# Kernel optimization log

Hardware: AMD Instinct MI355X
Metric: run time of the kernel (lower is better)

Reference implementation:

```python
import jax, jax.numpy as jnp
import numpy as np

MULTIRES = 6          # positional-encoding frequencies (get_embedder)
SKIP_LAYER = 4        # skip_in=(4,) in ImplicitNetwork
BETA = 100.0          # Softplus(beta=100)
INV_SQRT2 = float(1.0 / np.sqrt(2.0))
NUM_NETS = 64         # multi displacement networks (clusters)


def embed(x):
    """NeRF positional embedding: [x, sin(2^k x), cos(2^k x)] for k=0..MULTIRES-1.
    x: [N,3] -> [N, 3 + 3*2*MULTIRES] = [N,39]."""
    outs = [x]
    for i in range(MULTIRES):
        f = float(2.0 ** i)
        outs.append(jnp.sin(f * x))
        outs.append(jnp.cos(f * x))
    return jnp.concatenate(outs, axis=-1)


def softplus100(x):
    # numerically stable softplus with beta=100
    return jnp.logaddexp(0.0, BETA * x) / BETA


def _forward(points,
             iW0, ib0, iW1, ib1, iW2, ib2, iW3, ib3, iW4, ib4,
             iW5, ib5, iW6, ib6, iW7, ib7, iW8, ib8,
             dW0, db0, dW1, db1, dW2, db2, dW3, db3,
             mW0, mb0, mW1, mb1, mW2, mb2):
    N = points.shape[0]
    inp = embed(points)  # [N,39]

    # ---- ImplicitNetwork: 9 linears, softplus(beta=100), skip concat at l=4 ----
    iWs = [iW0, iW1, iW2, iW3, iW4, iW5, iW6, iW7, iW8]
    ibs = [ib0, ib1, ib2, ib3, ib4, ib5, ib6, ib7, ib8]
    x = inp
    for l in range(9):
        if l == SKIP_LAYER:
            x = jnp.concatenate([x, inp], axis=1) * INV_SQRT2  # [N,473+39=512]
        x = x @ iWs[l].T + ibs[l]
        if l < 8:
            x = softplus100(x)
    sdf_feat = x  # [N,257] = sdf (1) + feature vector (256)

    # ---- DisplacementNetwork: 4 linears, ReLU on hidden, Tanh output ----
    xd = inp
    for W, b, last in ((dW0, db0, False), (dW1, db1, False), (dW2, db2, False), (dW3, db3, True)):
        xd = xd @ W.T + b
        xd = jnp.tanh(xd) if last else jax.nn.relu(xd)
    disp = xd  # [N,3]

    # ---- MultiDisplacementNetwork: batched per-cluster MLPs via bmm ----
    xm = inp.reshape(NUM_NETS, -1, inp.shape[1])  # [n, N/n, 39]
    xm = jax.nn.relu(jnp.einsum('nbi,noi->nbo', xm, mW0) + mb0[:, None, :])
    xm = jax.nn.relu(jnp.einsum('nbi,noi->nbo', xm, mW1) + mb1[:, None, :])
    xm = jnp.tanh(jnp.einsum('nbi,noi->nbo', xm, mW2) + mb2[:, None, :])
    mdisp = xm.reshape(N, 3)

    return jnp.concatenate([sdf_feat, disp, mdisp], axis=1)  # [N, 263]


def setup_inputs() -> dict:
    key = jax.random.key(0)
    ks = iter(jax.random.split(key, 80))
    N = 32768
    d = {}
    d['points'] = jax.random.uniform(next(ks), (N, 3), jnp.float32, -1.0, 1.0)

    def mk(out, inn):
        W = jax.random.normal(next(ks), (out, inn), jnp.float32) * (1.0 / np.sqrt(inn))
        b = jax.random.normal(next(ks), (out,), jnp.float32) * 0.01
        return W, b

    impl_shapes = [(512, 39), (512, 512), (512, 512), (473, 512), (512, 512),
                   (512, 512), (512, 512), (512, 512), (257, 512)]
    for l, (o, i) in enumerate(impl_shapes):
        d[f'iW{l}'], d[f'ib{l}'] = mk(o, i)

    disp_shapes = [(512, 39), (512, 512), (512, 512), (3, 512)]
    for l, (o, i) in enumerate(disp_shapes):
        d[f'dW{l}'], d[f'db{l}'] = mk(o, i)

    multi_shapes = [(128, 39), (128, 128), (3, 128)]
    for l, (o, i) in enumerate(multi_shapes):
        W = jax.random.normal(next(ks), (NUM_NETS, o, i), jnp.float32) * (1.0 / np.sqrt(i))
        b = jax.random.normal(next(ks), (NUM_NETS, o), jnp.float32) * 0.01
        d[f'mW{l}'], d[f'mb{l}'] = W, b
    return d


def reference(points,
              iW0, ib0, iW1, ib1, iW2, ib2, iW3, ib3, iW4, ib4,
              iW5, ib5, iW6, ib6, iW7, ib7, iW8, ib8,
              dW0, db0, dW1, db1, dW2, db2, dW3, db3,
              mW0, mb0, mW1, mb1, mW2, mb2):
    return _forward(points,
                    iW0, ib0, iW1, ib1, iW2, ib2, iW3, ib3, iW4, ib4,
                    iW5, ib5, iW6, ib6, iW7, ib7, iW8, ib8,
                    dW0, db0, dW1, db1, dW2, db2, dW3, db3,
                    mW0, mb0, mW1, mb1, mW2, mb2)
```

## Files before the change

### kernel.cpp

```cpp
#include <hip/hip_runtime.h>
#include <stdint.h>

typedef __attribute__((ext_vector_type(8))) short short8;
typedef __attribute__((ext_vector_type(4))) float floatx4;

#define INV_SQRT2F 0.70710678118654752440f

__device__ ushort g_wbuf[4259840];

__device__ __forceinline__ ushort f2bf(float f) {
    union { float f; uint32_t u; } c; c.f = f;
    uint32_t x = c.u;
    return (ushort)((x + 0x7fffu + ((x >> 16) & 1u)) >> 16);
}
__device__ __forceinline__ float softplus100(float x) {
    float z = 100.f * x;
    return fmaxf(x, 0.f) + __logf(1.f + __expf(-fabsf(z))) * 0.01f;
}
__device__ __forceinline__ int swz(int row, int col) {
    return (((col >> 3) ^ (row & 7)) << 3) | (col & 7);
}

struct Seg { const float* s; int off, nout, kw, k32, ttot, nclust; };
struct CvtAll { Seg seg[16]; };

__global__ void k_cvt(CvtAll c) {
    Seg sg = c.seg[blockIdx.y];
    ushort* d = g_wbuf + sg.off;
    const int pcs8 = sg.ttot * sg.k32 * 64;
    const int tot8 = pcs8 * sg.nclust;
    for (int i8 = blockIdx.x * blockDim.x + threadIdx.x; i8 < tot8;
         i8 += gridDim.x * blockDim.x) {
        int cl = i8 / pcs8;
        int r = i8 - cl * pcs8;
        int t = r / (sg.k32 * 64);
        int r2 = r - t * (sg.k32 * 64);
        int kc = r2 >> 6;
        int lane = r2 & 63;
        int n = t * 16 + (lane & 15);
        int kb = kc * 32 + (lane >> 4) * 8;
        const float* src = sg.s + (size_t)cl * sg.nout * sg.kw;
        short8 v = {0, 0, 0, 0, 0, 0, 0, 0};
        if (n < sg.nout) {
#pragma unroll
            for (int j = 0; j < 8; ++j) {
                int k = kb + j;
                if (k < sg.kw) v[j] = (short)f2bf(src[n * sg.kw + k]);
            }
        }
        *(short8*)(d + (size_t)i8 * 8) = v;
    }
}

template<int STRIDE>
__device__ void embed128(short* act, const float* pts, int row0, short* inp_sv) {
    for (int idx = threadIdx.x; idx < 128 * 64; idx += 1024) {
        int row = idx >> 6, col = idx & 63;
        float v = 0.f;
        if (col < 39) {
            int comp = (col < 3) ? col : (col - 3) % 3;
            float x = pts[(row0 + row) * 3 + comp];
            if (col < 3) v = x;
            else {
                int b = col - 3; int fi = b / 6; int r = b % 6;
                float a = x * (float)(1 << fi);
                v = (r < 3) ? __sinf(a) : __cosf(a);
            }
        }
        act[row * STRIDE + swz(row, col)] = (short)f2bf(v);
        if (inp_sv && col < 39) inp_sv[row * 40 + col] = (short)f2bf(v * INV_SQRT2F);
    }
}

template<int ACT, int STRIDE, int K>
__device__ void layer_mm(short* act, const ushort* __restrict__ Wf,
                         const float* __restrict__ bias, int Nout, float scale,
                         bool toLds, float* gOut, int gCol0, int gRow0)
{
    constexpr int K32 = K / 32;
    const int tid = threadIdx.x;
    const int wave = tid >> 6, lane = tid & 63;
    const int q = lane >> 4, li = lane & 15;
    const int Ttot = (Nout + 15) >> 4;

    floatx4 acc[2][8];
#pragma unroll
    for (int i = 0; i < 2; ++i)
#pragma unroll
        for (int m = 0; m < 8; ++m) acc[i][m] = (floatx4){0.f, 0.f, 0.f, 0.f};

    bool tv[2]; int nn[2]; const ushort* wb[2];
#pragma unroll
    for (int i = 0; i < 2; ++i) {
        int t = wave + 16 * i;
        tv[i] = t < Ttot;
        nn[i] = t * 16 + li;
        wb[i] = Wf + (size_t)t * K32 * 512 + lane * 8;
    }

    auto loadB = [&](int kc, short8* b) {
#pragma unroll
        for (int i = 0; i < 2; ++i) {
            short8 z = {0, 0, 0, 0, 0, 0, 0, 0};
            b[i] = tv[i] ? *(const short8*)(wb[i] + kc * 512) : z;
        }
    };
    auto step = [&](int kc, short8* b) {
        const int gq = kc * 4 + q;
#pragma unroll
        for (int h = 0; h < 2; ++h) {
            short8 afr[4];
#pragma unroll
            for (int m2 = 0; m2 < 4; ++m2) {
                int row = (h * 4 + m2) * 16 + li;
                afr[m2] = *(const short8*)&act[row * STRIDE + ((gq ^ (row & 7)) << 3)];
            }
#pragma unroll
            for (int i = 0; i < 2; ++i) {
                if (!tv[i]) continue;
#pragma unroll
                for (int m2 = 0; m2 < 4; ++m2)
                    acc[i][h * 4 + m2] = __builtin_amdgcn_mfma_f32_16x16x32_bf16(
                        afr[m2], b[i], acc[i][h * 4 + m2], 0, 0, 0);
            }
        }
    };

    short8 b0[2], b1[2];
    loadB(0, b0);
#pragma unroll
    for (int kc = 0; kc < K32; kc += 2) {
        if (kc + 1 < K32) loadB(kc + 1, b1);
        step(kc, b0);
        if (kc + 2 < K32) loadB(kc + 2, b0);
        if (kc + 1 < K32) step(kc + 1, b1);
    }
    __syncthreads();
#pragma unroll
    for (int i = 0; i < 2; ++i) {
        if (!tv[i]) continue;
        int n = nn[i];
        if (n < Nout) {
            float bs = bias[n];
#pragma unroll
            for (int m = 0; m < 8; ++m) {
                int rbase = m * 16 + q * 4;
#pragma unroll
                for (int r = 0; r < 4; ++r) {
                    float v = acc[i][m][r] + bs;
                    if (ACT == 1) v = softplus100(v);
                    else if (ACT == 2) v = fmaxf(v, 0.f);
                    else if (ACT == 3) v = tanhf(v);
                    v *= scale;
                    if (toLds) act[(rbase + r) * STRIDE + swz(rbase + r, n)] = (short)f2bf(v);
                    else gOut[(size_t)(gRow0 + rbase + r) * 263 + gCol0 + n] = v;
                }
            }
        }
    }
}

struct IP { int iw[9]; const float* ib[9]; };

__global__ __launch_bounds__(1024, 4) void k_impl(const float* __restrict__ pts,
                                                  IP p, float* __restrict__ out) {
    __shared__ short act[128 * 512];
    __shared__ short inp_sv[128 * 40];
    const int row0 = blockIdx.x * 128;
    embed128<512>(act, pts, row0, inp_sv);
    __syncthreads();
    layer_mm<1, 512, 64>(act, g_wbuf + p.iw[0], p.ib[0], 512, 1.f, true, nullptr, 0, 0);
    __syncthreads();
    layer_mm<1, 512, 512>(act, g_wbuf + p.iw[1], p.ib[1], 512, 1.f, true, nullptr, 0, 0);
    __syncthreads();
    layer_mm<1, 512, 512>(act, g_wbuf + p.iw[2], p.ib[2], 512, 1.f, true, nullptr, 0, 0);
    __syncthreads();
    layer_mm<1, 512, 512>(act, g_wbuf + p.iw[3], p.ib[3], 473, INV_SQRT2F, true, nullptr, 0, 0);
    for (int idx = threadIdx.x; idx < 128 * 64; idx += 1024) {
        int row = idx >> 6, col = idx & 63;
        if (col < 39) act[row * 512 + swz(row, 473 + col)] = inp_sv[row * 40 + col];
    }
    __syncthreads();
    layer_mm<1, 512, 512>(act, g_wbuf + p.iw[4], p.ib[4], 512, 1.f, true, nullptr, 0, 0);
    __syncthreads();
    layer_mm<1, 512, 512>(act, g_wbuf + p.iw[5], p.ib[5], 512, 1.f, true, nullptr, 0, 0);
    __syncthreads();
    layer_mm<1, 512, 512>(act, g_wbuf + p.iw[6], p.ib[6], 512, 1.f, true, nullptr, 0, 0);
    __syncthreads();
    layer_mm<1, 512, 512>(act, g_wbuf + p.iw[7], p.ib[7], 512, 1.f, true, nullptr, 0, 0);
    __syncthreads();
    layer_mm<0, 512, 512>(act, g_wbuf + p.iw[8], p.ib[8], 257, 1.f, false, out, 0, row0);
}

struct DMP { int dw[4]; const float* db[4]; int mw[3]; const float* mb[3]; };

__global__ __launch_bounds__(1024, 4) void k_dm(const float* __restrict__ pts,
                                                DMP p, float* __restrict__ out,
                                                int nbD, int rpc) {
    __shared__ short act[128 * 512];
    const int bid = blockIdx.x;
    if (bid < nbD) {
        const int row0 = bid * 128;
        embed128<512>(act, pts, row0, nullptr);
        __syncthreads();
        layer_mm<2, 512, 64>(act, g_wbuf + p.dw[0], p.db[0], 512, 1.f, true, nullptr, 0, 0);
        __syncthreads();
        layer_mm<2, 512, 512>(act, g_wbuf + p.dw[1], p.db[1], 512, 1.f, true, nullptr, 0, 0);
        __syncthreads();
        layer_mm<2, 512, 512>(act, g_wbuf + p.dw[2], p.db[2], 512, 1.f, true, nullptr, 0, 0);
        __syncthreads();
        layer_mm<3, 512, 512>(act, g_wbuf + p.dw[3], p.db[3], 3, 1.f, false, out, 257, row0);
    } else {
        const int row0 = (bid - nbD) * 128;
        const int c = row0 / rpc;
        const ushort* w0 = g_wbuf + p.mw[0] + c * 8192;
        const ushort* w1 = g_wbuf + p.mw[1] + c * 16384;
        const ushort* w2 = g_wbuf + p.mw[2] + c * 2048;
        embed128<128>(act, pts, row0, nullptr);
        __syncthreads();
        layer_mm<2, 128, 64>(act, w0, p.mb[0] + c * 128, 128, 1.f, true, nullptr, 0, 0);
        __syncthreads();
        layer_mm<2, 128, 128>(act, w1, p.mb[1] + c * 128, 128, 1.f, true, nullptr, 0, 0);
        __syncthreads();
        layer_mm<3, 128, 128>(act, w2, p.mb[2] + c * 3, 3, 1.f, false, out, 260, row0);
    }
}

extern "C" void kernel_launch(void* const* d_in, const int* in_sizes, int n_in,
                              void* d_out, int out_size, void* d_ws, size_t ws_size,
                              hipStream_t stream) {
    const float* pts = (const float*)d_in[0];
    float* out = (float*)d_out;
    const int N = in_sizes[0] / 3;
    const int nbI = N / 128;
    const int nbD = N / 128;
    const int nbM = N / 128;
    const int rpc = N / 64;

    const int iN[9] = {512, 512, 512, 473, 512, 512, 512, 512, 257};
    const int iK[9] = {39, 512, 512, 512, 512, 512, 512, 512, 512};
    const int dN[4] = {512, 512, 512, 3};
    const int dK[4] = {39, 512, 512, 512};
    const int mN[3] = {128, 128, 3};
    const int mK[3] = {39, 128, 128};

    CvtAll cv; IP ip; DMP dm;
    int off = 0, seg = 0;
    auto add_seg = [&](const float* src, int nout, int kw, int nclust) -> int {
        int k32 = ((kw + 31) & ~31) / 32;
        int ttot = (nout + 15) >> 4;
        cv.seg[seg].s = src; cv.seg[seg].off = off;
        cv.seg[seg].nout = nout; cv.seg[seg].kw = kw;
        cv.seg[seg].k32 = k32; cv.seg[seg].ttot = ttot; cv.seg[seg].nclust = nclust;
        int my = off;
        off += ttot * k32 * 512 * nclust;
        ++seg;
        return my;
    };
    for (int l = 0; l < 9; ++l) {
        ip.iw[l] = add_seg((const float*)d_in[1 + 2 * l], iN[l], iK[l], 1);
        ip.ib[l] = (const float*)d_in[2 + 2 * l];
    }
    for (int l = 0; l < 4; ++l) {
        dm.dw[l] = add_seg((const float*)d_in[19 + 2 * l], dN[l], dK[l], 1);
        dm.db[l] = (const float*)d_in[20 + 2 * l];
    }
    for (int l = 0; l < 3; ++l) {
        dm.mw[l] = add_seg((const float*)d_in[27 + 2 * l], mN[l], mK[l], 64);
        dm.mb[l] = (const float*)d_in[28 + 2 * l];
    }

    k_cvt<<<dim3(256, 16), 256, 0, stream>>>(cv);
    k_impl<<<nbI, 1024, 0, stream>>>(pts, ip, out);
    k_dm<<<nbD + nbM, 1024, 0, stream>>>(pts, dm, out, nbD, rpc);
}
```

Before: 459.0 us.

## Retile layer GEMM as 4x4 wave tiles with swapped MFMA operands and packed stores

```diff
diff --git a/kernel.cpp b/kernel.cpp
--- a/kernel.cpp
+++ b/kernel.cpp
@@ -3,6 +3,7 @@
 
 typedef __attribute__((ext_vector_type(8))) short short8;
 typedef __attribute__((ext_vector_type(4))) float floatx4;
+typedef __attribute__((ext_vector_type(2))) uint uint2v;
 
 #define INV_SQRT2F 0.70710678118654752440f
 
@@ -81,80 +82,102 @@
     const int tid = threadIdx.x;
     const int wave = tid >> 6, lane = tid & 63;
     const int q = lane >> 4, li = lane & 15;
+    const int tg = wave >> 1, mg = wave & 1;
     const int Ttot = (Nout + 15) >> 4;
 
-    floatx4 acc[2][8];
-#pragma unroll
-    for (int i = 0; i < 2; ++i)
-#pragma unroll
-        for (int m = 0; m < 8; ++m) acc[i][m] = (floatx4){0.f, 0.f, 0.f, 0.f};
-
-    bool tv[2]; int nn[2]; const ushort* wb[2];
-#pragma unroll
-    for (int i = 0; i < 2; ++i) {
-        int t = wave + 16 * i;
+    floatx4 acc[4][4];
+#pragma unroll
+    for (int i = 0; i < 4; ++i)
+#pragma unroll
+        for (int j = 0; j < 4; ++j) acc[i][j] = (floatx4){0.f, 0.f, 0.f, 0.f};
+
+    bool tv[4]; const ushort* wb[4];
+#pragma unroll
+    for (int i = 0; i < 4; ++i) {
+        int t = tg * 4 + i;
         tv[i] = t < Ttot;
-        nn[i] = t * 16 + li;
         wb[i] = Wf + (size_t)t * K32 * 512 + lane * 8;
     }
-
-    auto loadB = [&](int kc, short8* b) {
-#pragma unroll
-        for (int i = 0; i < 2; ++i) {
+    int rowoff[4], r7[4];
+#pragma unroll
+    for (int j = 0; j < 4; ++j) {
+        int row = (mg * 4 + j) * 16 + li;
+        rowoff[j] = row * STRIDE;
+        r7[j] = row & 7;
+    }
+
+    auto loadW = [&](int kc, short8* w) {
+#pragma unroll
+        for (int i = 0; i < 4; ++i) {
             short8 z = {0, 0, 0, 0, 0, 0, 0, 0};
-            b[i] = tv[i] ? *(const short8*)(wb[i] + kc * 512) : z;
+            w[i] = tv[i] ? *(const short8*)(wb[i] + kc * 512) : z;
         }
     };
-    auto step = [&](int kc, short8* b) {
+    auto step = [&](int kc, short8* w) {
         const int gq = kc * 4 + q;
 #pragma unroll
-        for (int h = 0; h < 2; ++h) {
-            short8 afr[4];
-#pragma unroll
-            for (int m2 = 0; m2 < 4; ++m2) {
-                int row = (h * 4 + m2) * 16 + li;
-                afr[m2] = *(const short8*)&act[row * STRIDE + ((gq ^ (row & 7)) << 3)];
-            }
-#pragma unroll
-            for (int i = 0; i < 2; ++i) {
-                if (!tv[i]) continue;
-#pragma unroll
-                for (int m2 = 0; m2 < 4; ++m2)
-                    acc[i][h * 4 + m2] = __builtin_amdgcn_mfma_f32_16x16x32_bf16(
-                        afr[m2], b[i], acc[i][h * 4 + m2], 0, 0, 0);
-            }
+        for (int j = 0; j < 4; ++j) {
+            short8 afr = *(const short8*)&act[rowoff[j] + ((gq ^ r7[j]) << 3)];
+#pragma unroll
+            for (int i = 0; i < 4; ++i)
+                acc[i][j] = __builtin_amdgcn_mfma_f32_16x16x32_bf16(w[i], afr, acc[i][j], 0, 0, 0);
         }
     };
 
-    short8 b0[2], b1[2];
-    loadB(0, b0);
+    short8 w0[4], w1[4];
+    loadW(0, w0);
 #pragma unroll
     for (int kc = 0; kc < K32; kc += 2) {
-        if (kc + 1 < K32) loadB(kc + 1, b1);
-        step(kc, b0);
-        if (kc + 2 < K32) loadB(kc + 2, b0);
-        if (kc + 1 < K32) step(kc + 1, b1);
-    }
-    __syncthreads();
-#pragma unroll
-    for (int i = 0; i < 2; ++i) {
+        if (kc + 1 < K32) loadW(kc + 1, w1);
+        step(kc, w0);
+        if (kc + 2 < K32) loadW(kc + 2, w0);
+        if (kc + 1 < K32) step(kc + 1, w1);
+    }
+    __syncthreads();
+#pragma unroll
+    for (int i = 0; i < 4; ++i) {
         if (!tv[i]) continue;
-        int n = nn[i];
-        if (n < Nout) {
-            float bs = bias[n];
-#pragma unroll
-            for (int m = 0; m < 8; ++m) {
-                int rbase = m * 16 + q * 4;
-#pragma unroll
-                for (int r = 0; r < 4; ++r) {
-                    float v = acc[i][m][r] + bs;
-                    if (ACT == 1) v = softplus100(v);
-                    else if (ACT == 2) v = fmaxf(v, 0.f);
-                    else if (ACT == 3) v = tanhf(v);
-                    v *= scale;
-                    if (toLds) act[(rbase + r) * STRIDE + swz(rbase + r, n)] = (short)f2bf(v);
-                    else gOut[(size_t)(gRow0 + rbase + r) * 263 + gCol0 + n] = v;
+        const int nb = (tg * 4 + i) * 16 + q * 4;
+        if (nb >= Nout) continue;
+        const bool fullN = (nb + 4) <= Nout;
+        float bs[4];
+        if (fullN) {
+            float4 b4 = *(const float4*)(bias + nb);
+            bs[0] = b4.x; bs[1] = b4.y; bs[2] = b4.z; bs[3] = b4.w;
+        } else {
+#pragma unroll
+            for (int r = 0; r < 4; ++r) bs[r] = (nb + r < Nout) ? bias[nb + r] : 0.f;
+        }
+#pragma unroll
+        for (int j = 0; j < 4; ++j) {
+            const int row = (mg * 4 + j) * 16 + li;
+            float v[4];
+#pragma unroll
+            for (int r = 0; r < 4; ++r) {
+                float x = acc[i][j][r] + bs[r];
+                if (ACT == 1) x = softplus100(x);
+                else if (ACT == 2) x = fmaxf(x, 0.f);
+                else if (ACT == 3) x = tanhf(x);
+                v[r] = x * scale;
+            }
+            if (toLds) {
+                if (fullN) {
+                    uint lo = (uint)f2bf(v[0]) | ((uint)f2bf(v[1]) << 16);
+                    uint hi = (uint)f2bf(v[2]) | ((uint)f2bf(v[3]) << 16);
+                    int g = (nb >> 3) ^ (row & 7);
+                    uint2v pk = {lo, hi};
+                    *(uint2v*)&act[row * STRIDE + (g << 3) + (nb & 7)] = pk;
+                } else {
+#pragma unroll
+                    for (int r = 0; r < 4; ++r)
+                        if (nb + r < Nout)
+                            act[row * STRIDE + swz(row, nb + r)] = (short)f2bf(v[r]);
                 }
+            } else {
+#pragma unroll
+                for (int r = 0; r < 4; ++r)
+                    if (nb + r < Nout)
+                        gOut[(size_t)(gRow0 + row) * 263 + gCol0 + nb + r] = v[r];
             }
         }
     }
@@ -164,7 +187,7 @@
 
 __global__ __launch_bounds__(1024, 4) void k_impl(const float* __restrict__ pts,
                                                   IP p, float* __restrict__ out) {
-    __shared__ short act[128 * 512];
+    __shared__ __align__(16) short act[128 * 512];
     __shared__ short inp_sv[128 * 40];
     const int row0 = blockIdx.x * 128;
     embed128<512>(act, pts, row0, inp_sv);
@@ -197,7 +220,7 @@
 __global__ __launch_bounds__(1024, 4) void k_dm(const float* __restrict__ pts,
                                                 DMP p, float* __restrict__ out,
                                                 int nbD, int rpc) {
-    __shared__ short act[128 * 512];
+    __shared__ __align__(16) short act[128 * 512];
     const int bid = blockIdx.x;
     if (bid < nbD) {
         const int row0 = bid * 128;
```

New measurement: 544.6 us. 18.7% more time.

## Halve block size, widen per-wave tiles, prefetch next layer weights across layers

Applied to the files above, without the earlier changes.

```diff
diff --git a/kernel.cpp b/kernel.cpp
--- a/kernel.cpp
+++ b/kernel.cpp
@@ -19,6 +19,11 @@
 }
 __device__ __forceinline__ int swz(int row, int col) {
     return (((col >> 3) ^ (row & 7)) << 3) | (col & 7);
+}
+__device__ __forceinline__ void sync_lds() {
+    asm volatile("s_waitcnt lgkmcnt(0)" ::: "memory");
+    __builtin_amdgcn_s_barrier();
+    asm volatile("" ::: "memory");
 }
 
 struct Seg { const float* s; int off, nout, kw, k32, ttot, nclust; };
@@ -54,7 +59,7 @@
 
 template<int STRIDE>
 __device__ void embed128(short* act, const float* pts, int row0, short* inp_sv) {
-    for (int idx = threadIdx.x; idx < 128 * 64; idx += 1024) {
+    for (int idx = threadIdx.x; idx < 128 * 64; idx += 512) {
         int row = idx >> 6, col = idx & 63;
         float v = 0.f;
         if (col < 39) {
@@ -72,40 +77,49 @@
     }
 }
 
-template<int ACT, int STRIDE, int K>
-__device__ void layer_mm(short* act, const ushort* __restrict__ Wf,
-                         const float* __restrict__ bias, int Nout, float scale,
-                         bool toLds, float* gOut, int gCol0, int gRow0)
+template<int ACT, int STRIDE, int K32>
+__device__ __forceinline__ void big_layer(
+    short* act, const ushort* __restrict__ Wf, const float* __restrict__ bias,
+    int Nout, float scale, bool toLds, float* gOut, int gCol0, int gRow0,
+    short8 (&w0)[4], short8 (&w1)[4],
+    const ushort* nextW, int nStrideT, int nTtot)
 {
-    constexpr int K32 = K / 32;
     const int tid = threadIdx.x;
     const int wave = tid >> 6, lane = tid & 63;
     const int q = lane >> 4, li = lane & 15;
     const int Ttot = (Nout + 15) >> 4;
 
-    floatx4 acc[2][8];
-#pragma unroll
-    for (int i = 0; i < 2; ++i)
+    floatx4 acc[4][8];
+#pragma unroll
+    for (int i = 0; i < 4; ++i)
 #pragma unroll
         for (int m = 0; m < 8; ++m) acc[i][m] = (floatx4){0.f, 0.f, 0.f, 0.f};
 
-    bool tv[2]; int nn[2]; const ushort* wb[2];
-#pragma unroll
-    for (int i = 0; i < 2; ++i) {
-        int t = wave + 16 * i;
+    bool tv[4]; const ushort* wb[4]; float bs[4];
+#pragma unroll
+    for (int i = 0; i < 4; ++i) {
+        int t = wave + 8 * i;
         tv[i] = t < Ttot;
-        nn[i] = t * 16 + li;
-        wb[i] = Wf + (size_t)t * K32 * 512 + lane * 8;
-    }
-
-    auto loadB = [&](int kc, short8* b) {
-#pragma unroll
-        for (int i = 0; i < 2; ++i) {
-            short8 z = {0, 0, 0, 0, 0, 0, 0, 0};
-            b[i] = tv[i] ? *(const short8*)(wb[i] + kc * 512) : z;
-        }
-    };
-    auto step = [&](int kc, short8* b) {
+        wb[i] = Wf + (size_t)t * (K32 * 512) + lane * 8;
+        int n = t * 16 + li;
+        bs[i] = (tv[i] && n < Nout) ? bias[n] : 0.f;
+    }
+
+    auto loadW = [&](int kc, short8 (&w)[4]) {
+#pragma unroll
+        for (int i = 0; i < 4; ++i)
+            if (tv[i]) w[i] = *(const short8*)(wb[i] + kc * 512);
+    };
+    auto loadNext = [&](int kc, short8 (&w)[4]) {
+        if (!nextW) return;
+#pragma unroll
+        for (int i = 0; i < 4; ++i) {
+            int t = wave + 8 * i;
+            if (t < nTtot)
+                w[i] = *(const short8*)(nextW + (size_t)t * nStrideT + kc * 512 + lane * 8);
+        }
+    };
+    auto step = [&](int kc, short8 (&w)[4]) {
         const int gq = kc * 4 + q;
 #pragma unroll
         for (int h = 0; h < 2; ++h) {
@@ -116,45 +130,109 @@
                 afr[m2] = *(const short8*)&act[row * STRIDE + ((gq ^ (row & 7)) << 3)];
             }
 #pragma unroll
-            for (int i = 0; i < 2; ++i) {
+            for (int i = 0; i < 4; ++i) {
                 if (!tv[i]) continue;
 #pragma unroll
                 for (int m2 = 0; m2 < 4; ++m2)
                     acc[i][h * 4 + m2] = __builtin_amdgcn_mfma_f32_16x16x32_bf16(
-                        afr[m2], b[i], acc[i][h * 4 + m2], 0, 0, 0);
-            }
-        }
-    };
-
-    short8 b0[2], b1[2];
-    loadB(0, b0);
+                        afr[m2], w[i], acc[i][h * 4 + m2], 0, 0, 0);
+            }
+        }
+    };
+
 #pragma unroll
     for (int kc = 0; kc < K32; kc += 2) {
-        if (kc + 1 < K32) loadB(kc + 1, b1);
-        step(kc, b0);
-        if (kc + 2 < K32) loadB(kc + 2, b0);
-        if (kc + 1 < K32) step(kc + 1, b1);
-    }
-    __syncthreads();
-#pragma unroll
-    for (int i = 0; i < 2; ++i) {
+        step(kc, w0);
+        if (kc + 2 < K32) loadW(kc + 2, w0); else loadNext(0, w0);
+        step(kc + 1, w1);
+        if (kc + 3 < K32) loadW(kc + 3, w1); else loadNext(1, w1);
+    }
+    sync_lds();
+#pragma unroll
+    for (int i = 0; i < 4; ++i) {
         if (!tv[i]) continue;
-        int n = nn[i];
-        if (n < Nout) {
-            float bs = bias[n];
-#pragma unroll
-            for (int m = 0; m < 8; ++m) {
-                int rbase = m * 16 + q * 4;
-#pragma unroll
-                for (int r = 0; r < 4; ++r) {
-                    float v = acc[i][m][r] + bs;
-                    if (ACT == 1) v = softplus100(v);
-                    else if (ACT == 2) v = fmaxf(v, 0.f);
-                    else if (ACT == 3) v = tanhf(v);
-                    v *= scale;
-                    if (toLds) act[(rbase + r) * STRIDE + swz(rbase + r, n)] = (short)f2bf(v);
-                    else gOut[(size_t)(gRow0 + rbase + r) * 263 + gCol0 + n] = v;
-                }
+        int n = (wave + 8 * i) * 16 + li;
+        if (n >= Nout) continue;
+#pragma unroll
+        for (int m = 0; m < 8; ++m) {
+            int rbase = m * 16 + q * 4;
+#pragma unroll
+            for (int r = 0; r < 4; ++r) {
+                float v = acc[i][m][r] + bs[i];
+                if (ACT == 1) v = softplus100(v);
+                else if (ACT == 2) v = fmaxf(v, 0.f);
+                else if (ACT == 3) v = tanhf(v);
+                v *= scale;
+                if (toLds) act[(rbase + r) * STRIDE + swz(rbase + r, n)] = (short)f2bf(v);
+                else gOut[(size_t)(gRow0 + rbase + r) * 263 + gCol0 + n] = v;
+            }
+        }
+    }
+}
+
+template<int ACT, int K32>
+__device__ __forceinline__ void small_layer(
+    short* act, const ushort* __restrict__ Wf, const float* __restrict__ bias,
+    int Nout, bool toLds, float* gOut, int gCol0, int gRow0,
+    short8& w0, short8& w1, const ushort* nextW, int nStrideT, int nTtot)
+{
+    const int tid = threadIdx.x;
+    const int wave = tid >> 6, lane = tid & 63;
+    const int q = lane >> 4, li = lane & 15;
+    const int Ttot = (Nout + 15) >> 4;
+    const int t = wave;
+    const bool tv = t < Ttot;
+    const ushort* wb = Wf + (size_t)t * (K32 * 512) + lane * 8;
+    const int n = t * 16 + li;
+    const float bs = (tv && n < Nout) ? bias[n] : 0.f;
+
+    floatx4 acc[8];
+#pragma unroll
+    for (int m = 0; m < 8; ++m) acc[m] = (floatx4){0.f, 0.f, 0.f, 0.f};
+
+    auto loadW = [&](int kc, short8& w) {
+        if (tv) w = *(const short8*)(wb + kc * 512);
+    };
+    auto loadNext = [&](int kc, short8& w) {
+        if (nextW && t < nTtot)
+            w = *(const short8*)(nextW + (size_t)t * nStrideT + kc * 512 + lane * 8);
+    };
+    auto step = [&](int kc, short8& w) {
+        const int gq = kc * 4 + q;
+#pragma unroll
+        for (int h = 0; h < 2; ++h) {
+            short8 afr[4];
+#pragma unroll
+            for (int m2 = 0; m2 < 4; ++m2) {
+                int row = (h * 4 + m2) * 16 + li;
+                afr[m2] = *(const short8*)&act[row * 128 + ((gq ^ (row & 7)) << 3)];
+            }
+            if (tv)
+#pragma unroll
+                for (int m2 = 0; m2 < 4; ++m2)
+                    acc[h * 4 + m2] = __builtin_amdgcn_mfma_f32_16x16x32_bf16(
+                        afr[m2], w, acc[h * 4 + m2], 0, 0, 0);
+        }
+    };
+#pragma unroll
+    for (int kc = 0; kc < K32; kc += 2) {
+        step(kc, w0);
+        if (kc + 2 < K32) loadW(kc + 2, w0); else loadNext(0, w0);
+        step(kc + 1, w1);
+        if (kc + 3 < K32) loadW(kc + 3, w1); else loadNext(1, w1);
+    }
+    sync_lds();
+    if (tv && n < Nout) {
+#pragma unroll
+        for (int m = 0; m < 8; ++m) {
+            int rbase = m * 16 + q * 4;
+#pragma unroll
+            for (int r = 0; r < 4; ++r) {
+                float v = acc[m][r] + bs;
+                if (ACT == 2) v = fmaxf(v, 0.f);
+                else if (ACT == 3) v = tanhf(v);
+                if (toLds) act[(rbase + r) * 128 + swz(rbase + r, n)] = (short)f2bf(v);
+                else gOut[(size_t)(gRow0 + rbase + r) * 263 + gCol0 + n] = v;
             }
         }
     }
@@ -162,67 +240,106 @@
 
 struct IP { int iw[9]; const float* ib[9]; };
 
-__global__ __launch_bounds__(1024, 4) void k_impl(const float* __restrict__ pts,
-                                                  IP p, float* __restrict__ out) {
-    __shared__ short act[128 * 512];
+__global__ __launch_bounds__(512, 2) void k_impl(const float* __restrict__ pts,
+                                                 IP p, float* __restrict__ out) {
+    __shared__ __align__(16) short act[128 * 512];
     __shared__ short inp_sv[128 * 40];
     const int row0 = blockIdx.x * 128;
+    const int wave = threadIdx.x >> 6, lane = threadIdx.x & 63;
+
+    short8 w0[4], w1[4];
+#pragma unroll
+    for (int i = 0; i < 4; ++i) {
+        const ushort* b = g_wbuf + p.iw[0] + ((wave + 8 * i) * (2 * 512)) + lane * 8;
+        w0[i] = *(const short8*)b;
+        w1[i] = *(const short8*)(b + 512);
+    }
     embed128<512>(act, pts, row0, inp_sv);
-    __syncthreads();
-    layer_mm<1, 512, 64>(act, g_wbuf + p.iw[0], p.ib[0], 512, 1.f, true, nullptr, 0, 0);
-    __syncthreads();
-    layer_mm<1, 512, 512>(act, g_wbuf + p.iw[1], p.ib[1], 512, 1.f, true, nullptr, 0, 0);
-    __syncthreads();
-    layer_mm<1, 512, 512>(act, g_wbuf + p.iw[2], p.ib[2], 512, 1.f, true, nullptr, 0, 0);
-    __syncthreads();
-    layer_mm<1, 512, 512>(act, g_wbuf + p.iw[3], p.ib[3], 473, INV_SQRT2F, true, nullptr, 0, 0);
-    for (int idx = threadIdx.x; idx < 128 * 64; idx += 1024) {
+    sync_lds();
+    big_layer<1, 512, 2>(act, g_wbuf + p.iw[0], p.ib[0], 512, 1.f, true, nullptr, 0, 0,
+                         w0, w1, g_wbuf + p.iw[1], 8192, 32);
+    sync_lds();
+    big_layer<1, 512, 16>(act, g_wbuf + p.iw[1], p.ib[1], 512, 1.f, true, nullptr, 0, 0,
+                          w0, w1, g_wbuf + p.iw[2], 8192, 32);
+    sync_lds();
+    big_layer<1, 512, 16>(act, g_wbuf + p.iw[2], p.ib[2], 512, 1.f, true, nullptr, 0, 0,
+                          w0, w1, g_wbuf + p.iw[3], 8192, 32);
+    sync_lds();
+    big_layer<1, 512, 16>(act, g_wbuf + p.iw[3], p.ib[3], 473, INV_SQRT2F, true, nullptr, 0, 0,
+                          w0, w1, g_wbuf + p.iw[4], 8192, 32);
+    for (int idx = threadIdx.x; idx < 128 * 64; idx += 512) {
         int row = idx >> 6, col = idx & 63;
         if (col < 39) act[row * 512 + swz(row, 473 + col)] = inp_sv[row * 40 + col];
     }
-    __syncthreads();
-    layer_mm<1, 512, 512>(act, g_wbuf + p.iw[4], p.ib[4], 512, 1.f, true, nullptr, 0, 0);
-    __syncthreads();
-    layer_mm<1, 512, 512>(act, g_wbuf + p.iw[5], p.ib[5], 512, 1.f, true, nullptr, 0, 0);
-    __syncthreads();
-    layer_mm<1, 512, 512>(act, g_wbuf + p.iw[6], p.ib[6], 512, 1.f, true, nullptr, 0, 0);
-    __syncthreads();
-    layer_mm<1, 512, 512>(act, g_wbuf + p.iw[7], p.ib[7], 512, 1.f, true, nullptr, 0, 0);
-    __syncthreads();
-    layer_mm<0, 512, 512>(act, g_wbuf + p.iw[8], p.ib[8], 257, 1.f, false, out, 0, row0);
+    sync_lds();
+    big_layer<1, 512, 16>(act, g_wbuf + p.iw[4], p.ib[4], 512, 1.f, true, nullptr, 0, 0,
+                          w0, w1, g_wbuf + p.iw[5], 8192, 32);
+    sync_lds();
+    big_layer<1, 512, 16>(act, g_wbuf + p.iw[5], p.ib[5], 512, 1.f, true, nullptr, 0, 0,
+                          w0, w1, g_wbuf + p.iw[6], 8192, 32);
+    sync_lds();
+    big_layer<1, 512, 16>(act, g_wbuf + p.iw[6], p.ib[6], 512, 1.f, true, nullptr, 0, 0,
+                          w0, w1, g_wbuf + p.iw[7], 8192, 32);
+    sync_lds();
+    big_layer<1, 512, 16>(act, g_wbuf + p.iw[7], p.ib[7], 512, 1.f, true, nullptr, 0, 0,
+                          w0, w1, g_wbuf + p.iw[8], 8192, 17);
+    sync_lds();
+    big_layer<0, 512, 16>(act, g_wbuf + p.iw[8], p.ib[8], 257, 1.f, false, out, 0, row0,
+                          w0, w1, nullptr, 0, 0);
 }
 
 struct DMP { int dw[4]; const float* db[4]; int mw[3]; const float* mb[3]; };
 
-__global__ __launch_bounds__(1024, 4) void k_dm(const float* __restrict__ pts,
-                                                DMP p, float* __restrict__ out,
-                                                int nbD, int rpc) {
-    __shared__ short act[128 * 512];
+__global__ __launch_bounds__(512, 2) void k_dm(const float* __restrict__ pts,
+                                               DMP p, float* __restrict__ out,
+                                               int nbD, int rpc) {
+    __shared__ __align__(16) short act[128 * 512];
     const int bid = blockIdx.x;
+    const int wave = threadIdx.x >> 6, lane = threadIdx.x & 63;
     if (bid < nbD) {
         const int row0 = bid * 128;
+        short8 w0[4], w1[4];
+#pragma unroll
+        for (int i = 0; i < 4; ++i) {
+            const ushort* b = g_wbuf + p.dw[0] + ((wave + 8 * i) * (2 * 512)) + lane * 8;
+            w0[i] = *(const short8*)b;
+            w1[i] = *(const short8*)(b + 512);
+        }
         embed128<512>(act, pts, row0, nullptr);
-        __syncthreads();
-        layer_mm<2, 512, 64>(act, g_wbuf + p.dw[0], p.db[0], 512, 1.f, true, nullptr, 0, 0);
-        __syncthreads();
-        layer_mm<2, 512, 512>(act, g_wbuf + p.dw[1], p.db[1], 512, 1.f, true, nullptr, 0, 0);
-        __syncthreads();
-        layer_mm<2, 512, 512>(act, g_wbuf + p.dw[2], p.db[2], 512, 1.f, true, nullptr, 0, 0);
-        __syncthreads();
-        layer_mm<3, 512, 512>(act, g_wbuf + p.dw[3], p.db[3], 3, 1.f, false, out, 257, row0);
+        sync_lds();
+        big_layer<2, 512, 2>(act, g_wbuf + p.dw[0], p.db[0], 512, 1.f, true, nullptr, 0, 0,
+                             w0, w1, g_wbuf + p.dw[1], 8192, 32);
+        sync_lds();
+        big_layer<2, 512, 16>(act, g_wbuf + p.dw[1], p.db[1], 512, 1.f, true, nullptr, 0, 0,
+                              w0, w1, g_wbuf + p.dw[2], 8192, 32);
+        sync_lds();
+        big_layer<2, 512, 16>(act, g_wbuf + p.dw[2], p.db[2], 512, 1.f, true, nullptr, 0, 0,
+                              w0, w1, g_wbuf + p.dw[3], 8192, 1);
+        sync_lds();
+        big_layer<3, 512, 16>(act, g_wbuf + p.dw[3], p.db[3], 3, 1.f, false, out, 257, row0,
+                              w0, w1, nullptr, 0, 0);
     } else {
         const int row0 = (bid - nbD) * 128;
         const int c = row0 / rpc;
-        const ushort* w0 = g_wbuf + p.mw[0] + c * 8192;
-        const ushort* w1 = g_wbuf + p.mw[1] + c * 16384;
-        const ushort* w2 = g_wbuf + p.mw[2] + c * 2048;
+        const ushort* m0 = g_wbuf + p.mw[0] + c * 8192;
+        const ushort* m1 = g_wbuf + p.mw[1] + c * 16384;
+        const ushort* m2 = g_wbuf + p.mw[2] + c * 2048;
+        short8 w0, w1;
+        {
+            const ushort* b = m0 + (size_t)wave * (2 * 512) + lane * 8;
+            w0 = *(const short8*)b;
+            w1 = *(const short8*)(b + 512);
+        }
         embed128<128>(act, pts, row0, nullptr);
-        __syncthreads();
-        layer_mm<2, 128, 64>(act, w0, p.mb[0] + c * 128, 128, 1.f, true, nullptr, 0, 0);
-        __syncthreads();
-        layer_mm<2, 128, 128>(act, w1, p.mb[1] + c * 128, 128, 1.f, true, nullptr, 0, 0);
-        __syncthreads();
-        layer_mm<3, 128, 128>(act, w2, p.mb[2] + c * 3, 3, 1.f, false, out, 260, row0);
+        sync_lds();
+        small_layer<2, 2>(act, m0, p.mb[0] + c * 128, 128, true, nullptr, 0, 0,
+                          w0, w1, m1, 2048, 8);
+        sync_lds();
+        small_layer<2, 4>(act, m1, p.mb[1] + c * 128, 128, true, nullptr, 0, 0,
+                          w0, w1, m2, 2048, 1);
+        sync_lds();
+        small_layer<3, 4>(act, m2, p.mb[2] + c * 3, 3, false, out, 260, row0,
+                          w0, w1, nullptr, 0, 0);
     }
 }
 
@@ -271,6 +388,6 @@
     }
 
     k_cvt<<<dim3(256, 16), 256, 0, stream>>>(cv);
-    k_impl<<<nbI, 1024, 0, stream>>>(pts, ip, out);
-    k_dm<<<nbD + nbM, 1024, 0, stream>>>(pts, dm, out, nbD, rpc);
-}
+    k_impl<<<nbI, 512, 0, stream>>>(pts, ip, out);
+    k_dm<<<nbD + nbM, 512, 0, stream>>>(pts, dm, out, nbD, rpc);
+}
```

Measured after the change: 801.7 us. 1.75x slower.
